# Kernel optimization log

Measured on AMD Instinct MI355X. Metric: run time of the kernel, lower is better.

## Reference

```python
import jax, jax.numpy as jnp
import numpy as np

B, NCOL, NCOND = 1024, 64, 64
NRODT, D, NEST, NFOREST, NHID, NCLASS = 1024, 4, 128, 100, 128, 10
EPS = 1e-5


def setup_inputs() -> dict:
    key = jax.random.key(0)
    ks = jax.random.split(key, 16)
    rng = np.random.default_rng(0)
    s = 0.1
    inp = {
        'x': jax.random.normal(ks[0], (B, NCOL), jnp.float32),
        # phi_1 numerical grouped conv: groups=NCOL, in_per_g=1, out_per_g=NCOND
        'w1': jax.random.normal(ks[1], (NCOL, 1, NCOND), jnp.float32) * s,
        'b1': jax.random.normal(ks[2], (NCOL * NCOND,), jnp.float32) * s,
        # rODTConstruction fixed permutation of the 4096 conditions
        'perm': jnp.asarray(rng.permutation(NCOND * NCOL), jnp.int32),
        'gn1_g': jnp.ones((NCOND * NCOL,), jnp.float32),
        'gn1_b': jnp.zeros((NCOND * NCOL,), jnp.float32),
        # phi_2 grouped convs: groups=NRODT, block D->D then D->1
        'w2a': jax.random.normal(ks[3], (NRODT, D, D), jnp.float32) * s,
        'b2a': jax.random.normal(ks[4], (NRODT * D,), jnp.float32) * s,
        'gn2_g': jnp.ones((NCOND * NCOL,), jnp.float32),
        'gn2_b': jnp.zeros((NCOND * NCOL,), jnp.float32),
        'w2b': jax.random.normal(ks[5], (NRODT, D, 1), jnp.float32) * s,
        'b2b': jax.random.normal(ks[6], (NRODT,), jnp.float32) * s,
        'E': jax.random.normal(ks[7], (NRODT, NHID), jnp.float32) * s,
        # eval-mode sample_without_replacement buffer: per-forest subset of rODTs
        'swr': jnp.asarray(np.argsort(rng.random((NFOREST, NRODT)), axis=-1)[:, :NEST], jnp.int32),
        'ln1_g': jnp.ones((NHID,), jnp.float32),
        'ln1_b': jnp.zeros((NHID,), jnp.float32),
        'lin1_w': jax.random.normal(ks[8], (NHID, NHID), jnp.float32) * s,
        'lin1_b': jax.random.normal(ks[9], (NHID,), jnp.float32) * s,
        'ln2_g': jnp.ones((NHID,), jnp.float32),
        'ln2_b': jnp.zeros((NHID,), jnp.float32),
        'lin2_w': jax.random.normal(ks[10], (NHID, NCLASS), jnp.float32) * s,
        'lin2_b': jax.random.normal(ks[11], (NCLASS,), jnp.float32) * s,
    }
    return inp


def _group_norm(v, g, gamma, beta):
    # v: (B, C), normalize within each of g channel groups (L=1 in the torch module)
    b, c = v.shape
    vg = v.reshape(b, g, c // g)
    mu = vg.mean(-1, keepdims=True)
    var = vg.var(-1, keepdims=True)
    vn = ((vg - mu) / jnp.sqrt(var + EPS)).reshape(b, c)
    return vn * gamma + beta


def _layer_norm(v, gamma, beta):
    mu = v.mean(-1, keepdims=True)
    var = v.var(-1, keepdims=True)
    return (v - mu) / jnp.sqrt(var + EPS) * gamma + beta


def reference(x, w1, b1, perm, gn1_g, gn1_b, w2a, b2a, gn2_g, gn2_b, w2b, b2b,
              E, swr, ln1_g, ln1_b, lin1_w, lin1_b, ln2_g, ln2_b, lin2_w, lin2_b):
    b = x.shape[0]
    # ConditionGeneration (numerical only): block-diag GEMV with in_per_group=1
    M = jax.nn.sigmoid(x[:, :, None] * w1[None, :, 0, :] + b1.reshape(NCOL, NCOND))  # (B, NCOL, NCOND)
    M = M.transpose(0, 2, 1)  # (B, NCOND, NCOL)
    # rODTConstruction: flatten + fixed permutation
    O = M.reshape(b, NCOND * NCOL)[:, perm]  # (B, 4096)
    # phi_2: GroupNorm -> grouped conv (D->D) -> ReLU -> GroupNorm -> grouped conv (D->1)
    h = _group_norm(O, NRODT, gn1_g, gn1_b).reshape(b, NRODT, D)
    h = jnp.einsum('bgi,gio->bgo', h, w2a) + b2a.reshape(NRODT, D)
    h = jax.nn.relu(h).reshape(b, NRODT * D)
    h = _group_norm(h, NRODT, gn2_g, gn2_b).reshape(b, NRODT, D)
    w = jnp.einsum('bgi,gio->bgo', h, w2b)[..., 0] + b2b  # (B, NRODT), n_head=1
    # forest construction: gather rODT subsets, softmax over estimators, weighted embed sum
    ws = jax.nn.softmax(w[:, swr], axis=-1)  # (B, NFOREST, NEST)
    Es = E[swr]  # (NFOREST, NEST, NHID)
    F = jnp.einsum('bfe,feh->bfh', ws, Es)  # (B, NFOREST, NHID)
    # phi_3 bagging MLP (eval mode: dropout = identity)
    z = _layer_norm(F, ln1_g, ln1_b)
    z = jax.nn.relu(z @ lin1_w + lin1_b)
    z = _layer_norm(z, ln2_g, ln2_b)
    y_hats = z @ lin2_w + lin2_b  # (B, NFOREST, NCLASS)
    return y_hats.mean(1)  # (B, NCLASS)
```

## Files before the change

kernel.cpp:

```cpp
#include <hip/hip_runtime.h>


#define B_      1024
#define NCOL_   64
#define NCOND_  64
#define NRODT_  1024
#define NEST_   128
#define NFOREST_ 100
#define NHID_   128
#define NCLASS_ 10
#define EPS_    1e-5f

typedef __bf16 bf16_t;
typedef bf16_t bf16x8 __attribute__((ext_vector_type(8)));
typedef bf16_t bf16x4 __attribute__((ext_vector_type(4)));
typedef float  f32x4  __attribute__((ext_vector_type(4)));

#define MFMA16(a,b,c) __builtin_amdgcn_mfma_f32_16x16x32_bf16(a,b,c,0,0,0)

#define EG_FRAGS   (NFOREST_*4*8*64)
#define W1_FRAGS   (4*8*64)
#define L2_FRAGS   (4*64)
#define ZPAD_      248

__global__ __launch_bounds__(256) void k_pre(
    const float* __restrict__ x, float* __restrict__ x_t,
    float* __restrict__ accp)
{
    int blk = blockIdx.x, tid = threadIdx.x;
    if (blk < 256) {
        int t = blk * 256 + tid;
        x_t[t] = x[(t & 1023) * NCOL_ + (t >> 10)];
    } else {
        int t = (blk - 256) * 256 + tid;
        if (t < B_ * NCLASS_) accp[t] = 0.f;
    }
}

__global__ __launch_bounds__(256) void k_main(
    const float* __restrict__ E,     const int*   __restrict__ swr,
    const float* __restrict__ lin1w, const float* __restrict__ lin2w,
    bf16_t* __restrict__ Eh,  bf16_t* __restrict__ El,
    bf16_t* __restrict__ Wh,  bf16_t* __restrict__ Wl,
    bf16_t* __restrict__ L2h, bf16_t* __restrict__ L2l,
    const float* __restrict__ x_t,  const float* __restrict__ w1,
    const float* __restrict__ b1,   const int*  __restrict__ perm,
    const float* __restrict__ gn1g, const float* __restrict__ gn1b,
    const float* __restrict__ w2a,  const float* __restrict__ b2a,
    const float* __restrict__ gn2g, const float* __restrict__ gn2b,
    const float* __restrict__ w2b,  const float* __restrict__ b2b,
    bf16_t* __restrict__ w_t)
{
    int blk = blockIdx.x, tid = threadIdx.x;
    if (blk < 800) {
        int t = blk * 256 + tid;
        int lane = t & 63, nn = (t >> 6) & 7, kk = (t >> 9) & 3, f = t >> 11;
        int q = lane >> 4, n = nn * 16 + (lane & 15);
        bf16x8 hi, lo;
#pragma unroll
        for (int j = 0; j < 8; ++j) {
            int e = kk * 32 + q * 8 + j;
            int r = swr[f * NEST_ + e];
            float v = E[r * NHID_ + n];
            bf16_t h = (bf16_t)v;
            hi[j] = h; lo[j] = (bf16_t)(v - (float)h);
        }
        *(bf16x8*)(Eh + (size_t)t * 8) = hi;
        *(bf16x8*)(El + (size_t)t * 8) = lo;
        return;
    }
    if (blk < 808) {
        int t = (blk - 800) * 256 + tid;
        int lane = t & 63, nn = (t >> 6) & 7, kk = t >> 9;
        int q = lane >> 4, n = nn * 16 + (lane & 15);
        bf16x8 hi, lo;
#pragma unroll
        for (int j = 0; j < 8; ++j) {
            int k = kk * 32 + q * 8 + j;
            float v = lin1w[k * NHID_ + n];
            bf16_t h = (bf16_t)v;
            hi[j] = h; lo[j] = (bf16_t)(v - (float)h);
        }
        *(bf16x8*)(Wh + t * 8) = hi;
        *(bf16x8*)(Wl + t * 8) = lo;
        return;
    }
    if (blk == 808) {
        int t = tid;
        int lane = t & 63, kk = t >> 6;
        int q = lane >> 4, n = lane & 15;
        bf16x8 hi, lo;
#pragma unroll
        for (int j = 0; j < 8; ++j) {
            int k = kk * 32 + q * 8 + j;
            float v = (n < NCLASS_) ? lin2w[k * NCLASS_ + n] : 0.f;
            bf16_t h = (bf16_t)v;
            hi[j] = h; lo[j] = (bf16_t)(v - (float)h);
        }
        *(bf16x8*)(L2h + t * 8) = hi;
        *(bf16x8*)(L2l + t * 8) = lo;
        return;
    }

    int g  = blk - 809;
    int bq = tid * 4;

    int4 p4 = ((const int4*)perm)[g];
    int col[4]  = { p4.x & 63, p4.y & 63, p4.z & 63, p4.w & 63 };
    int cond[4] = { p4.x >> 6, p4.y >> 6, p4.z >> 6, p4.w >> 6 };
    float w1v[4], b1v[4];
#pragma unroll
    for (int j = 0; j < 4; ++j) {
        w1v[j] = w1[col[j] * NCOND_ + cond[j]];
        b1v[j] = b1[col[j] * NCOND_ + cond[j]];
    }
    float4 g1  = ((const float4*)gn1g)[g];
    float4 o1  = ((const float4*)gn1b)[g];
    float4 ba  = ((const float4*)b2a)[g];
    float4 g2  = ((const float4*)gn2g)[g];
    float4 o2  = ((const float4*)gn2b)[g];
    float4 wb4 = ((const float4*)w2b)[g];
    float  bb  = b2b[g];
    float4 wa[4];
    const float4* w2a4 = (const float4*)w2a;
#pragma unroll
    for (int i = 0; i < 4; ++i) wa[i] = w2a4[g * 4 + i];

    float xv[4][4];
#pragma unroll
    for (int j = 0; j < 4; ++j) {
        float4 t = *(const float4*)&x_t[col[j] * B_ + bq];
        xv[j][0] = t.x; xv[j][1] = t.y; xv[j][2] = t.z; xv[j][3] = t.w;
    }

    bf16x4 outv;
#pragma unroll
    for (int bi = 0; bi < 4; ++bi) {
        float v[4];
#pragma unroll
        for (int j = 0; j < 4; ++j) {
            float t = xv[j][bi] * w1v[j] + b1v[j];
            v[j] = 1.0f / (1.0f + __expf(-t));
        }
        float mu = (v[0] + v[1] + v[2] + v[3]) * 0.25f;
        float var = 0.f;
#pragma unroll
        for (int j = 0; j < 4; ++j) { float d = v[j] - mu; var += d * d; }
        var *= 0.25f;
        float rs = rsqrtf(var + EPS_);
        float h[4];
        h[0] = (v[0] - mu) * rs * g1.x + o1.x;
        h[1] = (v[1] - mu) * rs * g1.y + o1.y;
        h[2] = (v[2] - mu) * rs * g1.z + o1.z;
        h[3] = (v[3] - mu) * rs * g1.w + o1.w;

        float4 a = ba;
#pragma unroll
        for (int i = 0; i < 4; ++i) {
            a.x += h[i] * wa[i].x; a.y += h[i] * wa[i].y;
            a.z += h[i] * wa[i].z; a.w += h[i] * wa[i].w;
        }
        float t2[4];
        t2[0] = fmaxf(a.x, 0.f); t2[1] = fmaxf(a.y, 0.f);
        t2[2] = fmaxf(a.z, 0.f); t2[3] = fmaxf(a.w, 0.f);

        float mu2 = (t2[0] + t2[1] + t2[2] + t2[3]) * 0.25f;
        float var2 = 0.f;
#pragma unroll
        for (int j = 0; j < 4; ++j) { float d = t2[j] - mu2; var2 += d * d; }
        var2 *= 0.25f;
        float rs2 = rsqrtf(var2 + EPS_);

        float wvv = bb;
        wvv += ((t2[0] - mu2) * rs2 * g2.x + o2.x) * wb4.x;
        wvv += ((t2[1] - mu2) * rs2 * g2.y + o2.y) * wb4.y;
        wvv += ((t2[2] - mu2) * rs2 * g2.z + o2.z) * wb4.z;
        wvv += ((t2[3] - mu2) * rs2 * g2.w + o2.w) * wb4.w;
        outv[bi] = (bf16_t)wvv;
    }
    *(bf16x4*)&w_t[(size_t)g * B_ + bq] = outv;
}

__global__ __launch_bounds__(256, 5) void k_forest(
    const bf16_t* __restrict__ w_t, const int* __restrict__ swr,
    const bf16_t* __restrict__ Eh,  const bf16_t* __restrict__ El,
    const bf16_t* __restrict__ Wh,  const bf16_t* __restrict__ Wl,
    const bf16_t* __restrict__ L2h, const bf16_t* __restrict__ L2l,
    const float* __restrict__ ln1g, const float* __restrict__ ln1b,
    const float* __restrict__ lin1b,
    const float* __restrict__ ln2g, const float* __restrict__ ln2b,
    float* __restrict__ accp)
{
    __shared__ bf16_t zsh[4][16 * ZPAD_];

    int tid  = threadIdx.x;
    int wid  = tid >> 6;
    int lane = tid & 63;
    int q    = lane >> 4;
    int mc   = lane & 15;

    int n    = blockIdx.x;
    int swiz = (n & 7) * 200 + (n >> 3);
    int f    = swiz >> 4;
    int bt   = swiz & 15;
    int b0   = bt * 64 + wid * 16;

    const int* swrf = swr + f * NEST_;
    bf16_t* zw = zsh[wid];

    float ex[4][8];
    float mx = -1e30f;
#pragma unroll
    for (int kk = 0; kk < 4; ++kk) {
        int4 r0 = *(const int4*)(swrf + kk * 32 + q * 8);
        int4 r1 = *(const int4*)(swrf + kk * 32 + q * 8 + 4);
        int rr[8] = { r0.x, r0.y, r0.z, r0.w, r1.x, r1.y, r1.z, r1.w };
#pragma unroll
        for (int j = 0; j < 8; ++j) {
            float v = (float)w_t[rr[j] * B_ + b0 + mc];
            ex[kk][j] = v;
            mx = fmaxf(mx, v);
        }
    }
    mx = fmaxf(mx, __shfl_xor(mx, 16));
    mx = fmaxf(mx, __shfl_xor(mx, 32));
    float s = 0.f;
#pragma unroll
    for (int kk = 0; kk < 4; ++kk)
#pragma unroll
        for (int j = 0; j < 8; ++j) { ex[kk][j] = __expf(ex[kk][j] - mx); s += ex[kk][j]; }
    s += __shfl_xor(s, 16);
    s += __shfl_xor(s, 32);
    float inv = 1.f / s;

    bf16x8 afr[4];
#pragma unroll
    for (int kk = 0; kk < 4; ++kk)
#pragma unroll
        for (int j = 0; j < 8; ++j) afr[kk][j] = (bf16_t)(ex[kk][j] * inv);

    f32x4 accF[8];
#pragma unroll
    for (int nn = 0; nn < 8; ++nn) accF[nn] = (f32x4){0.f, 0.f, 0.f, 0.f};
    const bf16x8* EHf = (const bf16x8*)Eh;
    const bf16x8* ELf = (const bf16x8*)El;
#pragma unroll
    for (int kk = 0; kk < 4; ++kk) {
        size_t bi = (size_t)(f * 4 + kk) * 8;
#pragma unroll
        for (int nn = 0; nn < 8; ++nn) {
            bf16x8 bh = EHf[(bi + nn) * 64 + lane];
            bf16x8 bl = ELf[(bi + nn) * 64 + lane];
            accF[nn] = MFMA16(afr[kk], bh, accF[nn]);
            accF[nn] = MFMA16(afr[kk], bl, accF[nn]);
        }
    }

    float mu[4], rs[4];
#pragma unroll
    for (int reg = 0; reg < 4; ++reg) {
        float ps = 0.f, pq = 0.f;
#pragma unroll
        for (int nn = 0; nn < 8; ++nn) { float v = accF[nn][reg]; ps += v; pq += v * v; }
#pragma unroll
        for (int o = 1; o <= 8; o <<= 1) { ps += __shfl_xor(ps, o); pq += __shfl_xor(pq, o); }
        float m_ = ps * (1.f / NHID_);
        mu[reg] = m_;
        rs[reg] = rsqrtf(pq * (1.f / NHID_) - m_ * m_ + EPS_);
    }
#pragma unroll
    for (int nn = 0; nn < 8; ++nn) {
        int c = nn * 16 + mc;
        float gv = ln1g[c], bv = ln1b[c];
#pragma unroll
        for (int reg = 0; reg < 4; ++reg)
            zw[(q * 4 + reg) * ZPAD_ + c] =
                (bf16_t)((accF[nn][reg] - mu[reg]) * rs[reg] * gv + bv);
    }

    bf16x8 a2[4];
#pragma unroll
    for (int kk = 0; kk < 4; ++kk)
        a2[kk] = *(const bf16x8*)&zw[mc * ZPAD_ + kk * 32 + q * 8];
    f32x4 accA[8];
#pragma unroll
    for (int nn = 0; nn < 8; ++nn) accA[nn] = (f32x4){0.f, 0.f, 0.f, 0.f};
    const bf16x8* WHf = (const bf16x8*)Wh;
    const bf16x8* WLf = (const bf16x8*)Wl;
#pragma unroll
    for (int kk = 0; kk < 4; ++kk) {
#pragma unroll
        for (int nn = 0; nn < 8; ++nn) {
            bf16x8 bh = WHf[(kk * 8 + nn) * 64 + lane];
            bf16x8 bl = WLf[(kk * 8 + nn) * 64 + lane];
            accA[nn] = MFMA16(a2[kk], bh, accA[nn]);
            accA[nn] = MFMA16(a2[kk], bl, accA[nn]);
        }
    }

#pragma unroll
    for (int nn = 0; nn < 8; ++nn) {
        float bv = lin1b[nn * 16 + mc];
#pragma unroll
        for (int reg = 0; reg < 4; ++reg)
            accA[nn][reg] = fmaxf(accA[nn][reg] + bv, 0.f);
    }
    float mu2[4], rs2[4];
#pragma unroll
    for (int reg = 0; reg < 4; ++reg) {
        float ps = 0.f, pq = 0.f;
#pragma unroll
        for (int nn = 0; nn < 8; ++nn) { float v = accA[nn][reg]; ps += v; pq += v * v; }
#pragma unroll
        for (int o = 1; o <= 8; o <<= 1) { ps += __shfl_xor(ps, o); pq += __shfl_xor(pq, o); }
        float m_ = ps * (1.f / NHID_);
        mu2[reg] = m_;
        rs2[reg] = rsqrtf(pq * (1.f / NHID_) - m_ * m_ + EPS_);
    }
#pragma unroll
    for (int nn = 0; nn < 8; ++nn) {
        int c = nn * 16 + mc;
        float gv = ln2g[c], bv = ln2b[c];
#pragma unroll
        for (int reg = 0; reg < 4; ++reg)
            zw[(q * 4 + reg) * ZPAD_ + c] =
                (bf16_t)((accA[nn][reg] - mu2[reg]) * rs2[reg] * gv + bv);
    }

    f32x4 accO = {0.f, 0.f, 0.f, 0.f};
    const bf16x8* LHf = (const bf16x8*)L2h;
    const bf16x8* LLf = (const bf16x8*)L2l;
#pragma unroll
    for (int kk = 0; kk < 4; ++kk) {
        bf16x8 a3 = *(const bf16x8*)&zw[mc * ZPAD_ + kk * 32 + q * 8];
        accO = MFMA16(a3, LHf[kk * 64 + lane], accO);
        accO = MFMA16(a3, LLf[kk * 64 + lane], accO);
    }
    if (mc < NCLASS_) {
#pragma unroll
        for (int reg = 0; reg < 4; ++reg)
            atomicAdd(&accp[(b0 + q * 4 + reg) * NCLASS_ + mc], accO[reg]);
    }
}

__global__ __launch_bounds__(256) void k_final(
    const float* __restrict__ accp, const float* __restrict__ lin2b,
    float* __restrict__ out)
{
    int i = blockIdx.x * 256 + threadIdx.x;
    if (i < B_ * NCLASS_) {
        int c = i % NCLASS_;
        out[i] = accp[i] * (1.f / NFOREST_) + lin2b[c];
    }
}

extern "C" void kernel_launch(void* const* d_in, const int* in_sizes, int n_in,
                              void* d_out, int out_size, void* d_ws, size_t ws_size,
                              hipStream_t stream)
{
    const float* x     = (const float*)d_in[0];
    const float* w1    = (const float*)d_in[1];
    const float* b1    = (const float*)d_in[2];
    const int*   perm  = (const int*)  d_in[3];
    const float* gn1g  = (const float*)d_in[4];
    const float* gn1b  = (const float*)d_in[5];
    const float* w2a   = (const float*)d_in[6];
    const float* b2a   = (const float*)d_in[7];
    const float* gn2g  = (const float*)d_in[8];
    const float* gn2b  = (const float*)d_in[9];
    const float* w2b   = (const float*)d_in[10];
    const float* b2b   = (const float*)d_in[11];
    const float* E     = (const float*)d_in[12];
    const int*   swr   = (const int*)  d_in[13];
    const float* ln1g  = (const float*)d_in[14];
    const float* ln1b  = (const float*)d_in[15];
    const float* lin1w = (const float*)d_in[16];
    const float* lin1b = (const float*)d_in[17];
    const float* ln2g  = (const float*)d_in[18];
    const float* ln2b  = (const float*)d_in[19];
    const float* lin2w = (const float*)d_in[20];
    const float* lin2b = (const float*)d_in[21];

    char* base = (char*)d_ws;
    bf16_t* w_t  = (bf16_t*)base;
    float*  x_t  = (float*)(base + 2u * 1024 * 1024);
    float*  accp = (float*)(base + 2u * 1024 * 1024 + 256 * 1024);
    bf16_t* Eh   = (bf16_t*)(base + 2u * 1024 * 1024 + 256 * 1024 + 64 * 1024);
    bf16_t* El   = Eh  + (size_t)EG_FRAGS * 8;
    bf16_t* Wh   = El  + (size_t)EG_FRAGS * 8;
    bf16_t* Wl   = Wh  + (size_t)W1_FRAGS * 8;
    bf16_t* L2h  = Wl  + (size_t)W1_FRAGS * 8;
    bf16_t* L2l  = L2h + (size_t)L2_FRAGS * 8;

    float* outp = (float*)d_out;

    k_pre<<<296, 256, 0, stream>>>(x, x_t, accp);

    k_main<<<1833, 256, 0, stream>>>(E, swr, lin1w, lin2w,
                                     Eh, El, Wh, Wl, L2h, L2l,
                                     x_t, w1, b1, perm, gn1g, gn1b,
                                     w2a, b2a, gn2g, gn2b, w2b, b2b, w_t);

    k_forest<<<NFOREST_ * 16, 256, 0, stream>>>(
        w_t, swr, Eh, El, Wh, Wl, L2h, L2l,
        ln1g, ln1b, lin1b, ln2g, ln2b, accp);

    k_final<<<(B_ * NCLASS_ + 255) / 256, 256, 0, stream>>>(
        accp, lin2b, outp);
}
```

Measured before the change: 151.0 us.

## Process two row tiles per wave and drop low-part split of gathered E

Each wave in the forest kernel now handles two 16-row M tiles instead of one. Every loaded B fragment (E, lin1, lin2) therefore feeds two MFMAs, and the grid shrinks to half as many blocks. The gathered embedding matrix is stored as a single bf16 copy instead of a hi/lo pair, which halves the E fragment traffic and the MFMAs for that GEMM. In exchange, precision drops for the softmax-weighted embedding sum, register pressure rises (launch bounds lowered from 5 to 3 waves), and shared padding is reduced to fit the doubled z buffers.

```diff
diff --git a/kernel.cpp b/kernel.cpp
--- a/kernel.cpp
+++ b/kernel.cpp
@@ -21,7 +21,7 @@
 #define EG_FRAGS   (NFOREST_*4*8*64)
 #define W1_FRAGS   (4*8*64)
 #define L2_FRAGS   (4*64)
-#define ZPAD_      248
+#define ZPAD_      136
 
 __global__ __launch_bounds__(256) void k_pre(
     const float* __restrict__ x, float* __restrict__ x_t,
@@ -40,7 +40,7 @@
 __global__ __launch_bounds__(256) void k_main(
     const float* __restrict__ E,     const int*   __restrict__ swr,
     const float* __restrict__ lin1w, const float* __restrict__ lin2w,
-    bf16_t* __restrict__ Eh,  bf16_t* __restrict__ El,
+    bf16_t* __restrict__ Eg,
     bf16_t* __restrict__ Wh,  bf16_t* __restrict__ Wl,
     bf16_t* __restrict__ L2h, bf16_t* __restrict__ L2l,
     const float* __restrict__ x_t,  const float* __restrict__ w1,
@@ -56,17 +56,14 @@
         int t = blk * 256 + tid;
         int lane = t & 63, nn = (t >> 6) & 7, kk = (t >> 9) & 3, f = t >> 11;
         int q = lane >> 4, n = nn * 16 + (lane & 15);
-        bf16x8 hi, lo;
+        bf16x8 hi;
 #pragma unroll
         for (int j = 0; j < 8; ++j) {
             int e = kk * 32 + q * 8 + j;
             int r = swr[f * NEST_ + e];
-            float v = E[r * NHID_ + n];
-            bf16_t h = (bf16_t)v;
-            hi[j] = h; lo[j] = (bf16_t)(v - (float)h);
-        }
-        *(bf16x8*)(Eh + (size_t)t * 8) = hi;
-        *(bf16x8*)(El + (size_t)t * 8) = lo;
+            hi[j] = (bf16_t)E[r * NHID_ + n];
+        }
+        *(bf16x8*)(Eg + (size_t)t * 8) = hi;
         return;
     }
     if (blk < 808) {
@@ -181,9 +178,9 @@
     *(bf16x4*)&w_t[(size_t)g * B_ + bq] = outv;
 }
 
-__global__ __launch_bounds__(256, 5) void k_forest(
+__global__ __launch_bounds__(256, 3) void k_forest(
     const bf16_t* __restrict__ w_t, const int* __restrict__ swr,
-    const bf16_t* __restrict__ Eh,  const bf16_t* __restrict__ El,
+    const bf16_t* __restrict__ Eg,
     const bf16_t* __restrict__ Wh,  const bf16_t* __restrict__ Wl,
     const bf16_t* __restrict__ L2h, const bf16_t* __restrict__ L2l,
     const float* __restrict__ ln1g, const float* __restrict__ ln1b,
@@ -191,7 +188,7 @@
     const float* __restrict__ ln2g, const float* __restrict__ ln2b,
     float* __restrict__ accp)
 {
-    __shared__ bf16_t zsh[4][16 * ZPAD_];
+    __shared__ bf16_t zsh[8][16 * ZPAD_];
 
     int tid  = threadIdx.x;
     int wid  = tid >> 6;
@@ -200,91 +197,101 @@
     int mc   = lane & 15;
 
     int n    = blockIdx.x;
-    int swiz = (n & 7) * 200 + (n >> 3);
-    int f    = swiz >> 4;
-    int bt   = swiz & 15;
-    int b0   = bt * 64 + wid * 16;
+    int swiz = (n & 7) * 100 + (n >> 3);
+    int f    = swiz >> 3;
+    int bt   = swiz & 7;
+    int b0   = bt * 128 + wid * 32;
 
     const int* swrf = swr + f * NEST_;
-    bf16_t* zw = zsh[wid];
-
-    float ex[4][8];
-    float mx = -1e30f;
-#pragma unroll
-    for (int kk = 0; kk < 4; ++kk) {
-        int4 r0 = *(const int4*)(swrf + kk * 32 + q * 8);
-        int4 r1 = *(const int4*)(swrf + kk * 32 + q * 8 + 4);
-        int rr[8] = { r0.x, r0.y, r0.z, r0.w, r1.x, r1.y, r1.z, r1.w };
-#pragma unroll
-        for (int j = 0; j < 8; ++j) {
-            float v = (float)w_t[rr[j] * B_ + b0 + mc];
-            ex[kk][j] = v;
-            mx = fmaxf(mx, v);
-        }
-    }
-    mx = fmaxf(mx, __shfl_xor(mx, 16));
-    mx = fmaxf(mx, __shfl_xor(mx, 32));
-    float s = 0.f;
-#pragma unroll
-    for (int kk = 0; kk < 4; ++kk)
-#pragma unroll
-        for (int j = 0; j < 8; ++j) { ex[kk][j] = __expf(ex[kk][j] - mx); s += ex[kk][j]; }
-    s += __shfl_xor(s, 16);
-    s += __shfl_xor(s, 32);
-    float inv = 1.f / s;
-
-    bf16x8 afr[4];
-#pragma unroll
-    for (int kk = 0; kk < 4; ++kk)
-#pragma unroll
-        for (int j = 0; j < 8; ++j) afr[kk][j] = (bf16_t)(ex[kk][j] * inv);
-
-    f32x4 accF[8];
-#pragma unroll
-    for (int nn = 0; nn < 8; ++nn) accF[nn] = (f32x4){0.f, 0.f, 0.f, 0.f};
-    const bf16x8* EHf = (const bf16x8*)Eh;
-    const bf16x8* ELf = (const bf16x8*)El;
+
+    bf16x8 afr[2][4];
+#pragma unroll
+    for (int mt = 0; mt < 2; ++mt) {
+        int bm = b0 + mt * 16 + mc;
+        float ex[4][8];
+        float mx = -1e30f;
+#pragma unroll
+        for (int kk = 0; kk < 4; ++kk) {
+            int4 r0 = *(const int4*)(swrf + kk * 32 + q * 8);
+            int4 r1 = *(const int4*)(swrf + kk * 32 + q * 8 + 4);
+            int rr[8] = { r0.x, r0.y, r0.z, r0.w, r1.x, r1.y, r1.z, r1.w };
+#pragma unroll
+            for (int j = 0; j < 8; ++j) {
+                float v = (float)w_t[rr[j] * B_ + bm];
+                ex[kk][j] = v;
+                mx = fmaxf(mx, v);
+            }
+        }
+        mx = fmaxf(mx, __shfl_xor(mx, 16));
+        mx = fmaxf(mx, __shfl_xor(mx, 32));
+        float s = 0.f;
+#pragma unroll
+        for (int kk = 0; kk < 4; ++kk)
+#pragma unroll
+            for (int j = 0; j < 8; ++j) { ex[kk][j] = __expf(ex[kk][j] - mx); s += ex[kk][j]; }
+        s += __shfl_xor(s, 16);
+        s += __shfl_xor(s, 32);
+        float inv = 1.f / s;
+#pragma unroll
+        for (int kk = 0; kk < 4; ++kk)
+#pragma unroll
+            for (int j = 0; j < 8; ++j) afr[mt][kk][j] = (bf16_t)(ex[kk][j] * inv);
+    }
+
+    f32x4 accF[2][8];
+#pragma unroll
+    for (int mt = 0; mt < 2; ++mt)
+#pragma unroll
+        for (int nn = 0; nn < 8; ++nn) accF[mt][nn] = (f32x4){0.f, 0.f, 0.f, 0.f};
+    const bf16x8* EGf = (const bf16x8*)Eg;
 #pragma unroll
     for (int kk = 0; kk < 4; ++kk) {
         size_t bi = (size_t)(f * 4 + kk) * 8;
 #pragma unroll
         for (int nn = 0; nn < 8; ++nn) {
-            bf16x8 bh = EHf[(bi + nn) * 64 + lane];
-            bf16x8 bl = ELf[(bi + nn) * 64 + lane];
-            accF[nn] = MFMA16(afr[kk], bh, accF[nn]);
-            accF[nn] = MFMA16(afr[kk], bl, accF[nn]);
-        }
-    }
-
-    float mu[4], rs[4];
-#pragma unroll
-    for (int reg = 0; reg < 4; ++reg) {
-        float ps = 0.f, pq = 0.f;
-#pragma unroll
-        for (int nn = 0; nn < 8; ++nn) { float v = accF[nn][reg]; ps += v; pq += v * v; }
-#pragma unroll
-        for (int o = 1; o <= 8; o <<= 1) { ps += __shfl_xor(ps, o); pq += __shfl_xor(pq, o); }
-        float m_ = ps * (1.f / NHID_);
-        mu[reg] = m_;
-        rs[reg] = rsqrtf(pq * (1.f / NHID_) - m_ * m_ + EPS_);
-    }
-#pragma unroll
-    for (int nn = 0; nn < 8; ++nn) {
-        int c = nn * 16 + mc;
-        float gv = ln1g[c], bv = ln1b[c];
-#pragma unroll
-        for (int reg = 0; reg < 4; ++reg)
-            zw[(q * 4 + reg) * ZPAD_ + c] =
-                (bf16_t)((accF[nn][reg] - mu[reg]) * rs[reg] * gv + bv);
-    }
-
-    bf16x8 a2[4];
-#pragma unroll
-    for (int kk = 0; kk < 4; ++kk)
-        a2[kk] = *(const bf16x8*)&zw[mc * ZPAD_ + kk * 32 + q * 8];
-    f32x4 accA[8];
-#pragma unroll
-    for (int nn = 0; nn < 8; ++nn) accA[nn] = (f32x4){0.f, 0.f, 0.f, 0.f};
+            bf16x8 bh = EGf[(bi + nn) * 64 + lane];
+            accF[0][nn] = MFMA16(afr[0][kk], bh, accF[0][nn]);
+            accF[1][nn] = MFMA16(afr[1][kk], bh, accF[1][nn]);
+        }
+    }
+
+#pragma unroll
+    for (int mt = 0; mt < 2; ++mt) {
+        bf16_t* zw = zsh[wid * 2 + mt];
+        float mu[4], rs[4];
+#pragma unroll
+        for (int reg = 0; reg < 4; ++reg) {
+            float ps = 0.f, pq = 0.f;
+#pragma unroll
+            for (int nn = 0; nn < 8; ++nn) { float v = accF[mt][nn][reg]; ps += v; pq += v * v; }
+#pragma unroll
+            for (int o = 1; o <= 8; o <<= 1) { ps += __shfl_xor(ps, o); pq += __shfl_xor(pq, o); }
+            float m_ = ps * (1.f / NHID_);
+            mu[reg] = m_;
+            rs[reg] = rsqrtf(pq * (1.f / NHID_) - m_ * m_ + EPS_);
+        }
+#pragma unroll
+        for (int nn = 0; nn < 8; ++nn) {
+            int c = nn * 16 + mc;
+            float gv = ln1g[c], bv = ln1b[c];
+#pragma unroll
+            for (int reg = 0; reg < 4; ++reg)
+                zw[(q * 4 + reg) * ZPAD_ + c] =
+                    (bf16_t)((accF[mt][nn][reg] - mu[reg]) * rs[reg] * gv + bv);
+        }
+    }
+
+    bf16x8 a2[2][4];
+#pragma unroll
+    for (int mt = 0; mt < 2; ++mt)
+#pragma unroll
+        for (int kk = 0; kk < 4; ++kk)
+            a2[mt][kk] = *(const bf16x8*)&zsh[wid * 2 + mt][mc * ZPAD_ + kk * 32 + q * 8];
+    f32x4 accA[2][8];
+#pragma unroll
+    for (int mt = 0; mt < 2; ++mt)
+#pragma unroll
+        for (int nn = 0; nn < 8; ++nn) accA[mt][nn] = (f32x4){0.f, 0.f, 0.f, 0.f};
     const bf16x8* WHf = (const bf16x8*)Wh;
     const bf16x8* WLf = (const bf16x8*)Wl;
 #pragma unroll
@@ -293,53 +300,67 @@
         for (int nn = 0; nn < 8; ++nn) {
             bf16x8 bh = WHf[(kk * 8 + nn) * 64 + lane];
             bf16x8 bl = WLf[(kk * 8 + nn) * 64 + lane];
-            accA[nn] = MFMA16(a2[kk], bh, accA[nn]);
-            accA[nn] = MFMA16(a2[kk], bl, accA[nn]);
-        }
-    }
-
-#pragma unroll
-    for (int nn = 0; nn < 8; ++nn) {
-        float bv = lin1b[nn * 16 + mc];
-#pragma unroll
-        for (int reg = 0; reg < 4; ++reg)
-            accA[nn][reg] = fmaxf(accA[nn][reg] + bv, 0.f);
-    }
-    float mu2[4], rs2[4];
-#pragma unroll
-    for (int reg = 0; reg < 4; ++reg) {
-        float ps = 0.f, pq = 0.f;
-#pragma unroll
-        for (int nn = 0; nn < 8; ++nn) { float v = accA[nn][reg]; ps += v; pq += v * v; }
-#pragma unroll
-        for (int o = 1; o <= 8; o <<= 1) { ps += __shfl_xor(ps, o); pq += __shfl_xor(pq, o); }
-        float m_ = ps * (1.f / NHID_);
-        mu2[reg] = m_;
-        rs2[reg] = rsqrtf(pq * (1.f / NHID_) - m_ * m_ + EPS_);
-    }
-#pragma unroll
-    for (int nn = 0; nn < 8; ++nn) {
-        int c = nn * 16 + mc;
-        float gv = ln2g[c], bv = ln2b[c];
-#pragma unroll
-        for (int reg = 0; reg < 4; ++reg)
-            zw[(q * 4 + reg) * ZPAD_ + c] =
-                (bf16_t)((accA[nn][reg] - mu2[reg]) * rs2[reg] * gv + bv);
-    }
-
-    f32x4 accO = {0.f, 0.f, 0.f, 0.f};
+            accA[0][nn] = MFMA16(a2[0][kk], bh, accA[0][nn]);
+            accA[0][nn] = MFMA16(a2[0][kk], bl, accA[0][nn]);
+            accA[1][nn] = MFMA16(a2[1][kk], bh, accA[1][nn]);
+            accA[1][nn] = MFMA16(a2[1][kk], bl, accA[1][nn]);
+        }
+    }
+
+#pragma unroll
+    for (int mt = 0; mt < 2; ++mt) {
+        bf16_t* zw = zsh[wid * 2 + mt];
+#pragma unroll
+        for (int nn = 0; nn < 8; ++nn) {
+            float bv = lin1b[nn * 16 + mc];
+#pragma unroll
+            for (int reg = 0; reg < 4; ++reg)
+                accA[mt][nn][reg] = fmaxf(accA[mt][nn][reg] + bv, 0.f);
+        }
+        float mu2[4], rs2[4];
+#pragma unroll
+        for (int reg = 0; reg < 4; ++reg) {
+            float ps = 0.f, pq = 0.f;
+#pragma unroll
+            for (int nn = 0; nn < 8; ++nn) { float v = accA[mt][nn][reg]; ps += v; pq += v * v; }
+#pragma unroll
+            for (int o = 1; o <= 8; o <<= 1) { ps += __shfl_xor(ps, o); pq += __shfl_xor(pq, o); }
+            float m_ = ps * (1.f / NHID_);
+            mu2[reg] = m_;
+            rs2[reg] = rsqrtf(pq * (1.f / NHID_) - m_ * m_ + EPS_);
+        }
+#pragma unroll
+        for (int nn = 0; nn < 8; ++nn) {
+            int c = nn * 16 + mc;
+            float gv = ln2g[c], bv = ln2b[c];
+#pragma unroll
+            for (int reg = 0; reg < 4; ++reg)
+                zw[(q * 4 + reg) * ZPAD_ + c] =
+                    (bf16_t)((accA[mt][nn][reg] - mu2[reg]) * rs2[reg] * gv + bv);
+        }
+    }
+
+    f32x4 accO[2] = { (f32x4){0.f,0.f,0.f,0.f}, (f32x4){0.f,0.f,0.f,0.f} };
     const bf16x8* LHf = (const bf16x8*)L2h;
     const bf16x8* LLf = (const bf16x8*)L2l;
 #pragma unroll
     for (int kk = 0; kk < 4; ++kk) {
-        bf16x8 a3 = *(const bf16x8*)&zw[mc * ZPAD_ + kk * 32 + q * 8];
-        accO = MFMA16(a3, LHf[kk * 64 + lane], accO);
-        accO = MFMA16(a3, LLf[kk * 64 + lane], accO);
+        bf16x8 lh = LHf[kk * 64 + lane];
+        bf16x8 ll = LLf[kk * 64 + lane];
+        bf16x8 a30 = *(const bf16x8*)&zsh[wid * 2 + 0][mc * ZPAD_ + kk * 32 + q * 8];
+        bf16x8 a31 = *(const bf16x8*)&zsh[wid * 2 + 1][mc * ZPAD_ + kk * 32 + q * 8];
+        accO[0] = MFMA16(a30, lh, accO[0]);
+        accO[0] = MFMA16(a30, ll, accO[0]);
+        accO[1] = MFMA16(a31, lh, accO[1]);
+        accO[1] = MFMA16(a31, ll, accO[1]);
     }
     if (mc < NCLASS_) {
 #pragma unroll
-        for (int reg = 0; reg < 4; ++reg)
-            atomicAdd(&accp[(b0 + q * 4 + reg) * NCLASS_ + mc], accO[reg]);
+        for (int mt = 0; mt < 2; ++mt)
+#pragma unroll
+            for (int reg = 0; reg < 4; ++reg)
+                atomicAdd(&accp[(b0 + mt * 16 + q * 4 + reg) * NCLASS_ + mc],
+                          accO[mt][reg]);
     }
 }
 
@@ -385,9 +406,8 @@
     bf16_t* w_t  = (bf16_t*)base;
     float*  x_t  = (float*)(base + 2u * 1024 * 1024);
     float*  accp = (float*)(base + 2u * 1024 * 1024 + 256 * 1024);
-    bf16_t* Eh   = (bf16_t*)(base + 2u * 1024 * 1024 + 256 * 1024 + 64 * 1024);
-    bf16_t* El   = Eh  + (size_t)EG_FRAGS * 8;
-    bf16_t* Wh   = El  + (size_t)EG_FRAGS * 8;
+    bf16_t* Eg   = (bf16_t*)(base + 2u * 1024 * 1024 + 256 * 1024 + 64 * 1024);
+    bf16_t* Wh   = Eg  + (size_t)EG_FRAGS * 8;
     bf16_t* Wl   = Wh  + (size_t)W1_FRAGS * 8;
     bf16_t* L2h  = Wl  + (size_t)W1_FRAGS * 8;
     bf16_t* L2l  = L2h + (size_t)L2_FRAGS * 8;
@@ -397,12 +417,12 @@
     k_pre<<<296, 256, 0, stream>>>(x, x_t, accp);
 
     k_main<<<1833, 256, 0, stream>>>(E, swr, lin1w, lin2w,
-                                     Eh, El, Wh, Wl, L2h, L2l,
+                                     Eg, Wh, Wl, L2h, L2l,
                                      x_t, w1, b1, perm, gn1g, gn1b,
                                      w2a, b2a, gn2g, gn2b, w2b, b2b, w_t);
 
-    k_forest<<<NFOREST_ * 16, 256, 0, stream>>>(
-        w_t, swr, Eh, El, Wh, Wl, L2h, L2l,
+    k_forest<<<NFOREST_ * 8, 256, 0, stream>>>(
+        w_t, swr, Eg, Wh, Wl, L2h, L2l,
         ln1g, ln1b, lin1b, ln2g, ln2b, accp);
 
     k_final<<<(B_ * NCLASS_ + 255) / 256, 256, 0, stream>>>(
```

Measured after the change: 158.0 us. 4.7% more time.
